# Optimization experiments

Measured on AMD Instinct MI355X. Metric: run time of the kernel, lower is better.

## Reference

```python
import jax, jax.numpy as jnp
import numpy as np

# RankPool1d config (from init_kwargs)
RANK = 8          # kth smallest (1-indexed, as in torch.kthvalue)
KERNEL_SIZE = 16
STRIDE = 1
PADDING = 8
PAD_VALUE = 0.0   # mode='constant'

L = 4_194_304


def setup_inputs() -> dict:
    key = jax.random.key(0)
    x = jax.random.normal(key, (L,), dtype=jnp.float32)
    return {"x": x}


def reference(x):
    # F.pad(input, (PADDING, PADDING), mode='constant', value=PAD_VALUE)
    p = jnp.pad(x, (PADDING, PADDING), mode="constant", constant_values=PAD_VALUE)
    # p.unfold(0, KERNEL_SIZE, STRIDE) -> [out_len, KERNEL_SIZE] overlapping windows
    out_len = (p.shape[0] - KERNEL_SIZE) // STRIDE + 1
    idx = jnp.arange(out_len)[:, None] * STRIDE + jnp.arange(KERNEL_SIZE)[None, :]
    windows = p[idx]  # [out_len, k]
    # kthvalue(k=RANK, dim=1): value and index (within window) of RANK-th smallest
    order = jnp.argsort(windows, axis=1)          # [out_len, k]
    sel = order[:, RANK - 1]                       # [out_len] window-local index
    values = jnp.take_along_axis(windows, sel[:, None], axis=1)[:, 0]  # [out_len]
    return values, sel.astype(jnp.int32)
```

## Files before the change

kernel.cpp:

```cpp
#include <hip/hip_runtime.h>


constexpr int L_IN    = 4194304;
constexpr int OUT_LEN = L_IN + 1;
constexpr int MOUT    = 16;
constexpr int TPB     = 256;
constexpr int OPB     = TPB * MOUT;

__global__ __launch_bounds__(TPB) void rankpool_kernel(const float* __restrict__ x,
                                                       float* __restrict__ dout) {
    __shared__ __align__(16) float lv[OPB];
    __shared__ __align__(16) float ls[OPB + 2];

    const int t    = threadIdx.x;
    const int blk  = blockIdx.x;
    const int o0   = (blk * TPB + t) * MOUT;
    const int base = o0 - 8;
    const bool lastBlock = (blk == (int)gridDim.x - 1);

    float w[32];
    if (base >= 0 && base + 32 <= L_IN) {
        const float4* p = reinterpret_cast<const float4*>(x + base);
        #pragma unroll
        for (int q = 0; q < 8; ++q) {
            float4 v = p[q];
            w[4*q+0] = v.x; w[4*q+1] = v.y; w[4*q+2] = v.z; w[4*q+3] = v.w;
        }
    } else {
        #pragma unroll
        for (int i = 0; i < 32; ++i) {
            int g = base + i;
            w[i] = (g >= 0 && g < L_IN) ? x[g] : 0.0f;
        }
    }

    int R[31];
    #pragma unroll
    for (int j = 0; j < 16; ++j) R[j] = j;
    #pragma unroll
    for (int j = 0; j < 16; ++j) {
        #pragma unroll
        for (int k = j + 1; k < 16; ++k) {
            int c = (w[k] < w[j]);
            R[j] += c;
            R[k] -= c;
        }
    }

    #pragma unroll
    for (int m = 0; m < MOUT; ++m) {
        int   sel = 0;
        float val = w[m];
        #pragma unroll
        for (int j = m; j < m + 16; ++j) {
            bool c = (R[j] == 7 + m);
            sel = c ? (j - m) : sel;
            val = c ? w[j]    : val;
        }
        if (!lastBlock) {
            lv[t * MOUT + m]     = val;
            ls[t * MOUT + m + 1] = (float)sel;
        } else if (o0 + m < OUT_LEN) {
            dout[o0 + m]           = val;
            dout[OUT_LEN + o0 + m] = (float)sel;
        }

        if (m < MOUT - 1) {
            const float wm = w[m];
            const float wn = w[m + 16];
            int s = 0;
            #pragma unroll
            for (int j = m + 1; j < m + 16; ++j) {
                R[j] += (int)(w[j] < wm);
                int c2 = (wn < w[j]);
                R[j] += c2;
                s    += c2;
            }
            R[m + 16] = 16 + m - s;
        }
    }

    if (!lastBlock) {
        __syncthreads();
        const int blockStart = blk * OPB;

        #pragma unroll
        for (int k = 0; k < 4; ++k) {
            int i = t + k * TPB;
            float4 v = *reinterpret_cast<const float4*>(&lv[4 * i]);
            *reinterpret_cast<float4*>(dout + blockStart + 4 * i) = v;
        }

        float* s0 = dout + OUT_LEN + blockStart;
        if (t < 3)  s0[t] = ls[t + 1];
        if (t == 3) s0[OPB - 1] = ls[OPB];
        #pragma unroll
        for (int k = 0; k < 4; ++k) {
            int p = t + k * TPB;
            if (p < (OPB - 4) / 4 + 1 - 1) {
                float4 v = *reinterpret_cast<const float4*>(&ls[4 + 4 * p]);
                *reinterpret_cast<float4*>(s0 + 3 + 4 * p) = v;
            }
        }
    }
}

extern "C" void kernel_launch(void* const* d_in, const int* in_sizes, int n_in,
                              void* d_out, int out_size, void* d_ws, size_t ws_size,
                              hipStream_t stream) {
    const float* x = (const float*)d_in[0];
    float* out = (float*)d_out;
    const int threads = (OUT_LEN + MOUT - 1) / MOUT;
    const int blocks  = (threads + TPB - 1) / TPB;
    rankpool_kernel<<<blocks, TPB, 0, stream>>>(x, out);
}
```

Baseline: 25.65 us.

## Transpose shared-memory staging layout and peel final output into dedicated block

Shared-memory staging now writes per-output results in a column-major [m][thread] layout, so the per-m writes are bank-conflict free, and the store phase gathers scalars back into float4 global writes. The lone trailing output element is computed by a dedicated extra block with a single thread. This removes the lastBlock branching from the main path. The cost is scattered scalar LDS reads during the write-out, which may themselves cause bank conflicts.

```diff
diff --git a/kernel.cpp b/kernel.cpp
--- a/kernel.cpp
+++ b/kernel.cpp
@@ -9,14 +9,44 @@
 
 __global__ __launch_bounds__(TPB) void rankpool_kernel(const float* __restrict__ x,
                                                        float* __restrict__ dout) {
-    __shared__ __align__(16) float lv[OPB];
-    __shared__ __align__(16) float ls[OPB + 2];
+    __shared__ float lv[MOUT * TPB];
+    __shared__ float ls[MOUT * TPB];
 
-    const int t    = threadIdx.x;
-    const int blk  = blockIdx.x;
+    const int t   = threadIdx.x;
+    const int blk = blockIdx.x;
+
+    if (blk == 1024) {
+        if (t == 0) {
+            float w[16];
+            #pragma unroll
+            for (int i = 0; i < 16; ++i) {
+                int g = L_IN - 8 + i;
+                w[i] = (g < L_IN) ? x[g] : 0.0f;
+            }
+            int R[16];
+            #pragma unroll
+            for (int j = 0; j < 16; ++j) R[j] = j;
+            #pragma unroll
+            for (int j = 0; j < 16; ++j)
+                #pragma unroll
+                for (int k = j + 1; k < 16; ++k) {
+                    int c = (w[k] < w[j]);
+                    R[j] += c; R[k] -= c;
+                }
+            int sel = 0; float val = w[0];
+            #pragma unroll
+            for (int j = 0; j < 16; ++j) {
+                bool c = (R[j] == 7);
+                sel = c ? j : sel; val = c ? w[j] : val;
+            }
+            dout[OUT_LEN - 1]     = val;
+            dout[2 * OUT_LEN - 1] = (float)sel;
+        }
+        return;
+    }
+
     const int o0   = (blk * TPB + t) * MOUT;
     const int base = o0 - 8;
-    const bool lastBlock = (blk == (int)gridDim.x - 1);
 
     float w[32];
     if (base >= 0 && base + 32 <= L_IN) {
@@ -57,13 +87,8 @@
             sel = c ? (j - m) : sel;
             val = c ? w[j]    : val;
         }
-        if (!lastBlock) {
-            lv[t * MOUT + m]     = val;
-            ls[t * MOUT + m + 1] = (float)sel;
-        } else if (o0 + m < OUT_LEN) {
-            dout[o0 + m]           = val;
-            dout[OUT_LEN + o0 + m] = (float)sel;
-        }
+        lv[m * TPB + t] = val;
+        ls[m * TPB + t] = (float)sel;
 
         if (m < MOUT - 1) {
             const float wm = w[m];
@@ -80,27 +105,35 @@
         }
     }
 
-    if (!lastBlock) {
-        __syncthreads();
-        const int blockStart = blk * OPB;
+    __syncthreads();
 
-        #pragma unroll
-        for (int k = 0; k < 4; ++k) {
-            int i = t + k * TPB;
-            float4 v = *reinterpret_cast<const float4*>(&lv[4 * i]);
-            *reinterpret_cast<float4*>(dout + blockStart + 4 * i) = v;
-        }
+    const int blockStart = blk * OPB;
 
-        float* s0 = dout + OUT_LEN + blockStart;
-        if (t < 3)  s0[t] = ls[t + 1];
-        if (t == 3) s0[OPB - 1] = ls[OPB];
-        #pragma unroll
-        for (int k = 0; k < 4; ++k) {
-            int p = t + k * TPB;
-            if (p < (OPB - 4) / 4 + 1 - 1) {
-                float4 v = *reinterpret_cast<const float4*>(&ls[4 + 4 * p]);
-                *reinterpret_cast<float4*>(s0 + 3 + 4 * p) = v;
-            }
+    #pragma unroll
+    for (int k = 0; k < 4; ++k) {
+        int p = 4 * (t + 256 * k);
+        float4 v;
+        v.x = lv[((p + 0) & 15) * TPB + ((p + 0) >> 4)];
+        v.y = lv[((p + 1) & 15) * TPB + ((p + 1) >> 4)];
+        v.z = lv[((p + 2) & 15) * TPB + ((p + 2) >> 4)];
+        v.w = lv[((p + 3) & 15) * TPB + ((p + 3) >> 4)];
+        *reinterpret_cast<float4*>(dout + blockStart + p) = v;
+    }
+
+    float* s0 = dout + OUT_LEN + blockStart;
+    if (t < 3)  s0[t] = ls[t * TPB];
+    if (t == 3) s0[OPB - 1] = ls[15 * TPB + 255];
+    #pragma unroll
+    for (int k = 0; k < 4; ++k) {
+        int q = t + 256 * k;
+        if (q < 1023) {
+            int p = 3 + 4 * q;
+            float4 v;
+            v.x = ls[((p + 0) & 15) * TPB + ((p + 0) >> 4)];
+            v.y = ls[((p + 1) & 15) * TPB + ((p + 1) >> 4)];
+            v.z = ls[((p + 2) & 15) * TPB + ((p + 2) >> 4)];
+            v.w = ls[((p + 3) & 15) * TPB + ((p + 3) >> 4)];
+            *reinterpret_cast<float4*>(s0 + p) = v;
         }
     }
 }
@@ -110,7 +143,5 @@
                               hipStream_t stream) {
     const float* x = (const float*)d_in[0];
     float* out = (float*)d_out;
-    const int threads = (OUT_LEN + MOUT - 1) / MOUT;
-    const int blocks  = (threads + TPB - 1) / TPB;
-    rankpool_kernel<<<blocks, TPB, 0, stream>>>(x, out);
+    rankpool_kernel<<<1025, TPB, 0, stream>>>(x, out);
 }
```

Result: faster. 23.38 us (-8.9%).

## Use 4 outputs per thread with wave-shuffle index stores instead of LDS staging

Applied to the files above, without the earlier changes.

Each thread now computes 4 outputs instead of 16, so the grid has four times as many threads and each holds fewer registers. The shared-memory staging and block barrier are removed: values go straight out as a float4, and the misaligned index array is written by packing the 4 selections into one word and pulling the neighbour's selections with a wave shuffle. The single extra final output is handled by the last thread. The cost is more redundant work per output, since the initial 16x16 rank computation is now amortised over only 4 windows instead of 16.

```diff
diff --git a/kernel.cpp b/kernel.cpp
--- a/kernel.cpp
+++ b/kernel.cpp
@@ -1,40 +1,37 @@
 #include <hip/hip_runtime.h>
 
 
-constexpr int L_IN    = 4194304;
-constexpr int OUT_LEN = L_IN + 1;
-constexpr int MOUT    = 16;
-constexpr int TPB     = 256;
-constexpr int OPB     = TPB * MOUT;
+constexpr int L_IN     = 4194304;
+constexpr int OUT_LEN  = L_IN + 1;
+constexpr int TPB      = 256;
+constexpr int NTHREADS = (OUT_LEN - 1) / 4;
+constexpr int NBLK     = NTHREADS / TPB;
 
 __global__ __launch_bounds__(TPB) void rankpool_kernel(const float* __restrict__ x,
                                                        float* __restrict__ dout) {
-    __shared__ __align__(16) float lv[OPB];
-    __shared__ __align__(16) float ls[OPB + 2];
+    const int t    = blockIdx.x * TPB + threadIdx.x;
+    const int lane = threadIdx.x & 63;
+    const int o0   = t * 4;
+    const int base = o0 - 8;
+    const bool isLast = (t == NTHREADS - 1);
 
-    const int t    = threadIdx.x;
-    const int blk  = blockIdx.x;
-    const int o0   = (blk * TPB + t) * MOUT;
-    const int base = o0 - 8;
-    const bool lastBlock = (blk == (int)gridDim.x - 1);
-
-    float w[32];
-    if (base >= 0 && base + 32 <= L_IN) {
+    float w[20];
+    if (base >= 0 && base + 20 <= L_IN) {
         const float4* p = reinterpret_cast<const float4*>(x + base);
         #pragma unroll
-        for (int q = 0; q < 8; ++q) {
+        for (int q = 0; q < 5; ++q) {
             float4 v = p[q];
             w[4*q+0] = v.x; w[4*q+1] = v.y; w[4*q+2] = v.z; w[4*q+3] = v.w;
         }
     } else {
         #pragma unroll
-        for (int i = 0; i < 32; ++i) {
+        for (int i = 0; i < 20; ++i) {
             int g = base + i;
             w[i] = (g >= 0 && g < L_IN) ? x[g] : 0.0f;
         }
     }
 
-    int R[31];
+    int R[20];
     #pragma unroll
     for (int j = 0; j < 16; ++j) R[j] = j;
     #pragma unroll
@@ -47,8 +44,10 @@
         }
     }
 
+    float va[4];
+    unsigned pk = 0u;
     #pragma unroll
-    for (int m = 0; m < MOUT; ++m) {
+    for (int m = 0; m < 4; ++m) {
         int   sel = 0;
         float val = w[m];
         #pragma unroll
@@ -57,15 +56,10 @@
             sel = c ? (j - m) : sel;
             val = c ? w[j]    : val;
         }
-        if (!lastBlock) {
-            lv[t * MOUT + m]     = val;
-            ls[t * MOUT + m + 1] = (float)sel;
-        } else if (o0 + m < OUT_LEN) {
-            dout[o0 + m]           = val;
-            dout[OUT_LEN + o0 + m] = (float)sel;
-        }
+        va[m] = val;
+        pk |= ((unsigned)sel) << (8 * m);
 
-        if (m < MOUT - 1) {
+        if (m < 3) {
             const float wm = w[m];
             const float wn = w[m + 16];
             int s = 0;
@@ -80,28 +74,45 @@
         }
     }
 
-    if (!lastBlock) {
-        __syncthreads();
-        const int blockStart = blk * OPB;
+    *reinterpret_cast<float4*>(dout + o0) = make_float4(va[0], va[1], va[2], va[3]);
 
+    unsigned pn = __shfl_down(pk, 1, 64);
+    float* s0 = dout + OUT_LEN;
+    if (lane < 63) {
+        float4 sv = make_float4((float)(pk >> 24),
+                                (float)( pn        & 0xffu),
+                                (float)((pn >>  8) & 0xffu),
+                                (float)((pn >> 16) & 0xffu));
+        *reinterpret_cast<float4*>(s0 + o0 + 3) = sv;
+    } else {
+        s0[o0 + 3] = (float)(pk >> 24);
+    }
+    if (lane == 0) {
+        s0[o0 + 0] = (float)( pk        & 0xffu);
+        s0[o0 + 1] = (float)((pk >>  8) & 0xffu);
+        s0[o0 + 2] = (float)((pk >> 16) & 0xffu);
+    }
+
+    if (isLast) {
+        const float wm = w[3], wn = w[19];
+        int s = 0;
         #pragma unroll
-        for (int k = 0; k < 4; ++k) {
-            int i = t + k * TPB;
-            float4 v = *reinterpret_cast<const float4*>(&lv[4 * i]);
-            *reinterpret_cast<float4*>(dout + blockStart + 4 * i) = v;
+        for (int j = 4; j < 19; ++j) {
+            R[j] += (int)(w[j] < wm);
+            int c2 = (wn < w[j]);
+            R[j] += c2;
+            s    += c2;
         }
-
-        float* s0 = dout + OUT_LEN + blockStart;
-        if (t < 3)  s0[t] = ls[t + 1];
-        if (t == 3) s0[OPB - 1] = ls[OPB];
+        R[19] = 19 - s;
+        int sel = 0; float val = w[4];
         #pragma unroll
-        for (int k = 0; k < 4; ++k) {
-            int p = t + k * TPB;
-            if (p < (OPB - 4) / 4 + 1 - 1) {
-                float4 v = *reinterpret_cast<const float4*>(&ls[4 + 4 * p]);
-                *reinterpret_cast<float4*>(s0 + 3 + 4 * p) = v;
-            }
+        for (int j = 4; j < 20; ++j) {
+            bool c = (R[j] == 11);
+            sel = c ? (j - 4) : sel;
+            val = c ? w[j]    : val;
         }
+        dout[OUT_LEN - 1]     = val;
+        dout[2 * OUT_LEN - 1] = (float)sel;
     }
 }
 
@@ -110,7 +121,5 @@
                               hipStream_t stream) {
     const float* x = (const float*)d_in[0];
     float* out = (float*)d_out;
-    const int threads = (OUT_LEN + MOUT - 1) / MOUT;
-    const int blocks  = (threads + TPB - 1) / TPB;
-    rankpool_kernel<<<blocks, TPB, 0, stream>>>(x, out);
+    rankpool_kernel<<<NBLK, TPB, 0, stream>>>(x, out);
 }
```

Result: slower. 27.35 us (+6.6%).
